# Optimization experiments

Measured on AMD Instinct MI355X. Metric: run time of the kernel, lower is better.

The kernel has to match this reference:

```python
import jax, jax.numpy as jnp
import numpy as np

TAU = 2.0
V_TH = 1.0
V_RESET = 0.0
BN_EPS = 1e-5
SG_ALPHA = 2.0  # spikingjelly ATan surrogate default

@jax.custom_vjp
def spike_fn(x):
    return (x >= 0.0).astype(x.dtype)

def _spike_fwd(x):
    return spike_fn(x), x

def _spike_bwd(x, g):
    # ATan surrogate: alpha/2 / (1 + (pi/2*alpha*x)^2)
    sg = (SG_ALPHA / 2.0) / (1.0 + (jnp.pi / 2.0 * SG_ALPHA * x) ** 2)
    return (g * sg,)

spike_fn.defvjp(_spike_fwd, _spike_bwd)

def lif_multistep(x_seq):
    # x_seq: [T, B, C]; decay_input=False, hard reset, detach_reset=True
    def step(v, xt):
        v = v - (v - V_RESET) / TAU + xt
        s = spike_fn(v - V_TH)
        sd = jax.lax.stop_gradient(s)
        v = (1.0 - sd) * v + sd * V_RESET
        return v, s
    v0 = jnp.zeros_like(x_seq[0])
    _, s_seq = jax.lax.scan(step, v0, x_seq)
    return s_seq

def bn_eval(x, gamma, beta, mean, var):
    # x: [T, B, C], normalize over channel C (eval-mode BN)
    inv = gamma * jax.lax.rsqrt(var + BN_EPS)
    return x * inv + (beta - mean * inv)

def setup_inputs() -> dict:
    key = jax.random.key(0)
    ks = jax.random.split(key, 8)
    B, T, Cin, C, K = 64, 200, 80, 1024, 7
    x = jax.random.normal(ks[0], (B, T, Cin), dtype=jnp.float32)
    pw_w = jax.random.normal(ks[1], (C, Cin), dtype=jnp.float32) * (1.0 / np.sqrt(Cin))
    pw_b = jnp.zeros((C,), dtype=jnp.float32)
    dw_w = jax.random.normal(ks[2], (C, K), dtype=jnp.float32) * (1.0 / np.sqrt(K))
    dw_b = jnp.zeros((C,), dtype=jnp.float32)
    bn1_gamma = jnp.ones((C,), dtype=jnp.float32)
    bn1_beta = jnp.zeros((C,), dtype=jnp.float32)
    bn1_mean = jnp.zeros((C,), dtype=jnp.float32)
    bn1_var = jnp.ones((C,), dtype=jnp.float32)
    lin_w = jax.random.normal(ks[3], (C, C), dtype=jnp.float32) * (1.0 / np.sqrt(C))
    bn2_gamma = jnp.ones((C,), dtype=jnp.float32)
    bn2_beta = jnp.zeros((C,), dtype=jnp.float32)
    bn2_mean = jnp.zeros((C,), dtype=jnp.float32)
    bn2_var = jnp.ones((C,), dtype=jnp.float32)
    return dict(x=x, pw_w=pw_w, pw_b=pw_b, dw_w=dw_w, dw_b=dw_b,
                bn1_gamma=bn1_gamma, bn1_beta=bn1_beta, bn1_mean=bn1_mean, bn1_var=bn1_var,
                lin_w=lin_w,
                bn2_gamma=bn2_gamma, bn2_beta=bn2_beta, bn2_mean=bn2_mean, bn2_var=bn2_var)

def reference(x, pw_w, pw_b, dw_w, dw_b,
              bn1_gamma, bn1_beta, bn1_mean, bn1_var,
              lin_w,
              bn2_gamma, bn2_beta, bn2_mean, bn2_var):
    # x: [B, T, Cin] -> trans1 -> [B, Cin, T]
    h = jnp.transpose(x, (0, 2, 1))
    # pointwise conv1d (kernel 1): [B, Cin, T] -> [B, C, T]
    h = jnp.einsum('bct,oc->bot', h, pw_w) + pw_b[None, :, None]
    # depthwise conv1d, kernel 7, same padding
    C = dw_w.shape[0]
    h = jax.lax.conv_general_dilated(
        h, dw_w[:, None, :], window_strides=(1,), padding=[(3, 3)],
        feature_group_count=C, dimension_numbers=('NCH', 'OIH', 'NCH'))
    h = h + dw_b[None, :, None]
    # trans2: [B, C, T] -> [T, B, C]
    h = jnp.transpose(h, (2, 0, 1))
    h = bn_eval(h, bn1_gamma, bn1_beta, bn1_mean, bn1_var)
    h = lif_multistep(h)
    # dropout1: eval mode -> identity
    h_res = h
    h = jnp.einsum('tbc,oc->tbo', h, lin_w)  # Linear, no bias
    h = bn_eval(h, bn2_gamma, bn2_beta, bn2_mean, bn2_var)
    h = lif_multistep(h)
    # dropout2: eval mode -> identity
    return h + h_res  # [T, B, C]
```

## Files before the change

### kernel.cpp

```cpp
#include <hip/hip_runtime.h>
#include <hip/hip_bf16.h>
#include <stdint.h>

#define B_    64
#define T_    200
#define CIN_  80
#define C_    1024
#define M_    (B_ * T_)
#define BCEL  (B_ * C_)

typedef __attribute__((ext_vector_type(4))) float f32x4;
typedef __attribute__((ext_vector_type(8))) _Float16 f16x8;
typedef __attribute__((ext_vector_type(4))) unsigned int u32x4;

__global__ __launch_bounds__(256) void gemm_abt(
    const float* __restrict__ A, const float* __restrict__ Bm,
    const float* __restrict__ bias, float* __restrict__ C,
    int M, int N, int K) {
  __shared__ float As[16][64];
  __shared__ float Bs[16][64];
  const int tid = threadIdx.x;
  const int tx = tid & 15;
  const int ty = tid >> 4;
  const int m0 = blockIdx.x * 64;
  const int n0 = blockIdx.y * 64;
  const int lr = tid >> 2;
  const int lc = (tid & 3) * 4;

  float acc[4][4] = {{0.f,0.f,0.f,0.f},{0.f,0.f,0.f,0.f},
                     {0.f,0.f,0.f,0.f},{0.f,0.f,0.f,0.f}};
  const float* Aro = A + (size_t)(m0 + lr) * K + lc;
  const float* Bro = Bm + (size_t)(n0 + lr) * K + lc;

  for (int k0 = 0; k0 < K; k0 += 16) {
    float4 a4 = *(const float4*)(Aro + k0);
    float4 b4 = *(const float4*)(Bro + k0);
    __syncthreads();
    As[lc + 0][lr] = a4.x; As[lc + 1][lr] = a4.y;
    As[lc + 2][lr] = a4.z; As[lc + 3][lr] = a4.w;
    Bs[lc + 0][lr] = b4.x; Bs[lc + 1][lr] = b4.y;
    Bs[lc + 2][lr] = b4.z; Bs[lc + 3][lr] = b4.w;
    __syncthreads();
#pragma unroll
    for (int kk = 0; kk < 16; ++kk) {
      float4 av = *(const float4*)&As[kk][ty * 4];
      float4 bv = *(const float4*)&Bs[kk][tx * 4];
      acc[0][0] = fmaf(av.x, bv.x, acc[0][0]);
      acc[0][1] = fmaf(av.x, bv.y, acc[0][1]);
      acc[0][2] = fmaf(av.x, bv.z, acc[0][2]);
      acc[0][3] = fmaf(av.x, bv.w, acc[0][3]);
      acc[1][0] = fmaf(av.y, bv.x, acc[1][0]);
      acc[1][1] = fmaf(av.y, bv.y, acc[1][1]);
      acc[1][2] = fmaf(av.y, bv.z, acc[1][2]);
      acc[1][3] = fmaf(av.y, bv.w, acc[1][3]);
      acc[2][0] = fmaf(av.z, bv.x, acc[2][0]);
      acc[2][1] = fmaf(av.z, bv.y, acc[2][1]);
      acc[2][2] = fmaf(av.z, bv.z, acc[2][2]);
      acc[2][3] = fmaf(av.z, bv.w, acc[2][3]);
      acc[3][0] = fmaf(av.w, bv.x, acc[3][0]);
      acc[3][1] = fmaf(av.w, bv.y, acc[3][1]);
      acc[3][2] = fmaf(av.w, bv.z, acc[3][2]);
      acc[3][3] = fmaf(av.w, bv.w, acc[3][3]);
    }
  }

  float bj[4] = {0.f, 0.f, 0.f, 0.f};
  if (bias) {
#pragma unroll
    for (int j = 0; j < 4; ++j) bj[j] = bias[n0 + tx * 4 + j];
  }
#pragma unroll
  for (int i = 0; i < 4; ++i) {
    int m = m0 + ty * 4 + i;
    float4 o4;
    o4.x = acc[i][0] + bj[0];
    o4.y = acc[i][1] + bj[1];
    o4.z = acc[i][2] + bj[2];
    o4.w = acc[i][3] + bj[3];
    *(float4*)&C[(size_t)m * N + n0 + tx * 4] = o4;
  }
}

__global__ __launch_bounds__(256) void dw_bn_lif(
    const float* __restrict__ p, const float* __restrict__ dw_w,
    const float* __restrict__ dw_b, const float* __restrict__ gam,
    const float* __restrict__ bet, const float* __restrict__ mu,
    const float* __restrict__ var, ushort* __restrict__ s1) {
  int gid = blockIdx.x * blockDim.x + threadIdx.x;
  int b = gid >> 10;
  int o = gid & 1023;

  float w[7];
#pragma unroll
  for (int k = 0; k < 7; ++k) w[k] = dw_w[o * 7 + k];
  float db = dw_b[o];
  float inv = (float)((double)gam[o] / sqrt((double)var[o] + 1e-5));
  float add = (float)((double)bet[o] - (double)mu[o] * (double)inv);

  const float* pp = p + (size_t)b * T_ * C_ + o;
  float win[14];
  win[0] = 0.f; win[1] = 0.f; win[2] = 0.f;
#pragma unroll
  for (int i = 0; i < 11; ++i) win[3 + i] = pp[(size_t)i * C_];

  float v = 0.f;
  size_t obase = (size_t)b * C_ + o;
  for (int c = 0; c < T_ / 8; ++c) {
    int t0 = c * 8;
    float nx[8];
#pragma unroll
    for (int j = 0; j < 8; ++j) {
      int tn = t0 + 11 + j;
      nx[j] = (tn < T_) ? pp[(size_t)tn * C_] : 0.f;
    }
#pragma unroll
    for (int s = 0; s < 8; ++s) {
      float u = db;
#pragma unroll
      for (int k = 0; k < 7; ++k) u = fmaf(w[k], win[s + k], u);
      u = fmaf(u, inv, add);
      v = fmaf(0.5f, v, u);
      bool sp = (v - 1.0f) >= 0.0f;
      s1[obase + (size_t)(t0 + s) * BCEL] = sp ? (ushort)0x3C00 : (ushort)0;
      v = sp ? 0.0f : v;
    }
#pragma unroll
    for (int i = 0; i < 6; ++i) win[i] = win[i + 8];
#pragma unroll
    for (int j = 0; j < 8; ++j) win[6 + j] = nx[j];
  }
}

__global__ __launch_bounds__(256) void split_w(
    const float* __restrict__ w, ushort* __restrict__ w0,
    ushort* __restrict__ w1, int n) {
  int i = blockIdx.x * 256 + threadIdx.x;
  if (i >= n) return;
  float x = w[i];
  union { _Float16 h; ushort u; } h0, h1;
  h0.h = (_Float16)x;
  if (fabsf(x) < 6.1035156e-5f) h0.u = 0;
  float r = x - (float)h0.h;
  h1.h = (_Float16)(r * 2048.0f);
  w0[i] = h0.u;
  w1[i] = h1.u;
}

#define BM 128
#define BN 128
#define BKg 32

__global__ __launch_bounds__(256) void gemm_mfma2(
    const ushort* __restrict__ A,
    const ushort* __restrict__ B0,
    const ushort* __restrict__ B1,
    float* __restrict__ Cout) {
  const int K = C_;
  const int N = C_;
  __shared__ __align__(16) ushort Ash[BM * BKg];
  __shared__ __align__(16) ushort Bsh[2][BN * BKg];

  const int tid  = threadIdx.x;
  const int lane = tid & 63;
  const int wm = ((tid >> 6) >> 1) * 64;
  const int wn = ((tid >> 6) & 1) * 64;

  int lin = blockIdx.x;
  int qq = gridDim.x >> 3;
  int wg = (lin & 7) * qq + (lin >> 3);
  const int m0 = (wg >> 3) * BM;
  const int n0 = (wg & 7) * BN;

  const int r0 = tid >> 2, kc0 = (tid & 3) * 8;
  const int r1 = (tid + 256) >> 2, kc1 = ((tid + 256) & 3) * 8;

  f32x4 acc[4][4] = {};

  for (int k0 = 0; k0 < K; k0 += BKg) {
    __syncthreads();
    {
      const ushort* s0 = A + (size_t)(m0 + r0) * K + k0 + kc0;
      const ushort* s1p = A + (size_t)(m0 + r1) * K + k0 + kc1;
      __builtin_amdgcn_global_load_lds(
          (const __attribute__((address_space(1))) uint32_t*)s0,
          (__attribute__((address_space(3))) uint32_t*)&Ash[tid * 8], 16, 0, 0);
      __builtin_amdgcn_global_load_lds(
          (const __attribute__((address_space(1))) uint32_t*)s1p,
          (__attribute__((address_space(3))) uint32_t*)&Ash[(tid + 256) * 8], 16, 0, 0);
    }
#pragma unroll
    for (int s = 0; s < 2; ++s) {
      const ushort* Bp = (s == 0) ? B0 : B1;
      const ushort* s0 = Bp + (size_t)(n0 + r0) * K + k0 + kc0;
      const ushort* s1p = Bp + (size_t)(n0 + r1) * K + k0 + kc1;
      __builtin_amdgcn_global_load_lds(
          (const __attribute__((address_space(1))) uint32_t*)s0,
          (__attribute__((address_space(3))) uint32_t*)&Bsh[s][tid * 8], 16, 0, 0);
      __builtin_amdgcn_global_load_lds(
          (const __attribute__((address_space(1))) uint32_t*)s1p,
          (__attribute__((address_space(3))) uint32_t*)&Bsh[s][(tid + 256) * 8], 16, 0, 0);
    }
    __syncthreads();

    const int fr = lane & 15;
    const int k8 = (lane >> 4) * 8;
    union HU { f16x8 h; u32x4 u; };
    f16x8 af[4], a2f[4];
#pragma unroll
    for (int m = 0; m < 4; ++m) {
      HU t;
      t.h = *(const f16x8*)&Ash[(wm + m * 16 + fr) * BKg + k8];
      af[m] = t.h;
      t.u &= 0x10001000u;
      a2f[m] = t.h;
    }
    f16x8 b0f[4], b1f[4];
#pragma unroll
    for (int n = 0; n < 4; ++n) {
      b0f[n] = *(const f16x8*)&Bsh[0][(wn + n * 16 + fr) * BKg + k8];
      b1f[n] = *(const f16x8*)&Bsh[1][(wn + n * 16 + fr) * BKg + k8];
    }
#pragma unroll
    for (int m = 0; m < 4; ++m)
#pragma unroll
      for (int n = 0; n < 4; ++n) {
        acc[m][n] = __builtin_amdgcn_mfma_f32_16x16x32_f16(
            af[m], b0f[n], acc[m][n], 0, 0, 0);
        acc[m][n] = __builtin_amdgcn_mfma_f32_16x16x32_f16(
            a2f[m], b1f[n], acc[m][n], 0, 0, 0);
      }
  }

  const int ccol = lane & 15;
  const int crow = (lane >> 4) * 4;
#pragma unroll
  for (int m = 0; m < 4; ++m)
#pragma unroll
    for (int n = 0; n < 4; ++n)
#pragma unroll
      for (int j = 0; j < 4; ++j) {
        int row = m0 + wm + m * 16 + crow + j;
        int col = n0 + wn + n * 16 + ccol;
        Cout[(size_t)row * N + col] = acc[m][n][j];
      }
}

__global__ __launch_bounds__(256) void bn_lif_add(
    const float* __restrict__ y, const ushort* __restrict__ s1b,
    const float* __restrict__ gam, const float* __restrict__ bet,
    const float* __restrict__ mu, const float* __restrict__ var,
    float* __restrict__ out) {
  int gid = blockIdx.x * blockDim.x + threadIdx.x;
  int o = gid & 1023;

  float inv = (float)((double)gam[o] / sqrt((double)var[o] + 1e-5));
  float add = (float)((double)bet[o] - (double)mu[o] * (double)inv);

  float v = 0.f;
  size_t base = (size_t)gid;
  float yv[8]; ushort sv[8];
#pragma unroll
  for (int j = 0; j < 8; ++j) {
    yv[j] = y[base + (size_t)j * BCEL];
    sv[j] = s1b[base + (size_t)j * BCEL];
  }
  for (int c = 0; c < T_ / 8; ++c) {
    int t0 = c * 8;
    float yn[8] = {0,0,0,0,0,0,0,0}; ushort sn[8] = {0,0,0,0,0,0,0,0};
    if (c + 1 < T_ / 8) {
#pragma unroll
      for (int j = 0; j < 8; ++j) {
        size_t idx = base + (size_t)(t0 + 8 + j) * BCEL;
        yn[j] = y[idx];
        sn[j] = s1b[idx];
      }
    }
#pragma unroll
    for (int j = 0; j < 8; ++j) {
      float u = fmaf(yv[j], inv, add);
      v = fmaf(0.5f, v, u);
      bool sp = (v - 1.0f) >= 0.0f;
      float s1v = sv[j] ? 1.0f : 0.0f;
      out[base + (size_t)(t0 + j) * BCEL] = (sp ? 1.0f : 0.0f) + s1v;
      v = sp ? 0.0f : v;
    }
#pragma unroll
    for (int j = 0; j < 8; ++j) { yv[j] = yn[j]; sv[j] = sn[j]; }
  }
}

extern "C" void kernel_launch(void* const* d_in, const int* in_sizes, int n_in,
                              void* d_out, int out_size, void* d_ws,
                              size_t ws_size, hipStream_t stream) {
  const float* x     = (const float*)d_in[0];
  const float* pw_w  = (const float*)d_in[1];
  const float* pw_b  = (const float*)d_in[2];
  const float* dw_w  = (const float*)d_in[3];
  const float* dw_b  = (const float*)d_in[4];
  const float* bn1g  = (const float*)d_in[5];
  const float* bn1b  = (const float*)d_in[6];
  const float* bn1m  = (const float*)d_in[7];
  const float* bn1v  = (const float*)d_in[8];
  const float* lin_w = (const float*)d_in[9];
  const float* bn2g  = (const float*)d_in[10];
  const float* bn2b  = (const float*)d_in[11];
  const float* bn2m  = (const float*)d_in[12];
  const float* bn2v  = (const float*)d_in[13];

  char* wsb  = (char*)d_ws;
  char* outb = (char*)d_out;
  const size_t PB  = (size_t)M_ * C_ * 4;
  const size_t SBB = (size_t)M_ * C_ * 2;
  const size_t WB  = (size_t)C_ * C_ * 2;

  float* p = (float*)d_ws;

  const bool primary = ws_size >= PB + SBB;
  ushort* spikes = primary ? (ushort*)(wsb + PB) : (ushort*)d_out;
  ushort* w0  = primary ? (ushort*)outb : (ushort*)(wsb + SBB);
  ushort* w1s = w0 + (size_t)C_ * C_;
  ushort* Sgemm = primary ? spikes : (ushort*)d_ws;
  float* ybuf = primary ? (float*)d_ws : (float*)d_out;

  dim3 pw_grid(M_ / 64, C_ / 64);
  gemm_abt<<<pw_grid, 256, 0, stream>>>(x, pw_w, pw_b, p, M_, C_, CIN_);

  dw_bn_lif<<<BCEL / 256, 256, 0, stream>>>(p, dw_w, dw_b, bn1g, bn1b, bn1m,
                                            bn1v, spikes);

  if (!primary)
    hipMemcpyAsync(d_ws, d_out, SBB, hipMemcpyDeviceToDevice, stream);

  split_w<<<(C_ * C_ + 255) / 256, 256, 0, stream>>>(lin_w, w0, w1s, C_ * C_);

  gemm_mfma2<<<(M_ / BM) * (C_ / BN), 256, 0, stream>>>(Sgemm, w0, w1s, ybuf);

  bn_lif_add<<<BCEL / 256, 256, 0, stream>>>(ybuf, Sgemm, bn2g, bn2b, bn2m,
                                             bn2v, (float*)d_out);
}
```

Baseline: 160.0 us.

## Double-buffer LDS in MFMA GEMM with XOR swizzle and prefetch in pointwise GEMM

The split-fp16 MFMA GEMM now uses two LDS buffers. It issues global-to-LDS loads for the next K tile before the MFMAs of the current tile, which removes one barrier per iteration and overlaps memory with compute. It also applies an XOR swizzle to the k offset on both the write and read side, meant to reduce LDS bank conflicts. The fp32 pointwise GEMM register-prefetches the next A/B float4 before the inner FMA loop. The cost is double the LDS footprint (48KB), which may limit occupancy.

```diff
diff --git a/kernel.cpp b/kernel.cpp
--- a/kernel.cpp
+++ b/kernel.cpp
@@ -32,15 +32,20 @@
   const float* Aro = A + (size_t)(m0 + lr) * K + lc;
   const float* Bro = Bm + (size_t)(n0 + lr) * K + lc;
 
+  float4 a4 = *(const float4*)(Aro);
+  float4 b4 = *(const float4*)(Bro);
+
   for (int k0 = 0; k0 < K; k0 += 16) {
-    float4 a4 = *(const float4*)(Aro + k0);
-    float4 b4 = *(const float4*)(Bro + k0);
     __syncthreads();
     As[lc + 0][lr] = a4.x; As[lc + 1][lr] = a4.y;
     As[lc + 2][lr] = a4.z; As[lc + 3][lr] = a4.w;
     Bs[lc + 0][lr] = b4.x; Bs[lc + 1][lr] = b4.y;
     Bs[lc + 2][lr] = b4.z; Bs[lc + 3][lr] = b4.w;
     __syncthreads();
+    if (k0 + 16 < K) {
+      a4 = *(const float4*)(Aro + k0 + 16);
+      b4 = *(const float4*)(Bro + k0 + 16);
+    }
 #pragma unroll
     for (int kk = 0; kk < 16; ++kk) {
       float4 av = *(const float4*)&As[kk][ty * 4];
@@ -150,15 +155,14 @@
 #define BN 128
 #define BKg 32
 
-__global__ __launch_bounds__(256) void gemm_mfma2(
+__global__ __launch_bounds__(256) void gemm_mfma2p(
     const ushort* __restrict__ A,
     const ushort* __restrict__ B0,
     const ushort* __restrict__ B1,
     float* __restrict__ Cout) {
   const int K = C_;
   const int N = C_;
-  __shared__ __align__(16) ushort Ash[BM * BKg];
-  __shared__ __align__(16) ushort Bsh[2][BN * BKg];
+  __shared__ __align__(16) ushort lds[2][3][BM * BKg];
 
   const int tid  = threadIdx.x;
   const int lane = tid & 63;
@@ -171,55 +175,59 @@
   const int m0 = (wg >> 3) * BM;
   const int n0 = (wg & 7) * BN;
 
-  const int r0 = tid >> 2, kc0 = (tid & 3) * 8;
-  const int r1 = (tid + 256) >> 2, kc1 = ((tid + 256) & 3) * 8;
+  const int r0 = tid >> 2, r1 = r0 + 64;
+  const int kc = (tid & 3) * 8;
+  const int ks = kc ^ (((tid >> 3) & 3) << 3);
+
+  const int fr = lane & 15;
+  const int k8 = (lane >> 4) * 8;
+  const int k8s = k8 ^ (((fr >> 1) & 3) << 3);
 
   f32x4 acc[4][4] = {};
 
+#define STAGE(bufi, kk0)                                                       \
+  do {                                                                         \
+    __builtin_amdgcn_global_load_lds(                                          \
+        (const __attribute__((address_space(1))) uint32_t*)(A + (size_t)(m0 + r0) * K + (kk0) + ks),  \
+        (__attribute__((address_space(3))) uint32_t*)&lds[bufi][0][tid * 8], 16, 0, 0);               \
+    __builtin_amdgcn_global_load_lds(                                          \
+        (const __attribute__((address_space(1))) uint32_t*)(A + (size_t)(m0 + r1) * K + (kk0) + ks),  \
+        (__attribute__((address_space(3))) uint32_t*)&lds[bufi][0][(tid + 256) * 8], 16, 0, 0);       \
+    __builtin_amdgcn_global_load_lds(                                          \
+        (const __attribute__((address_space(1))) uint32_t*)(B0 + (size_t)(n0 + r0) * K + (kk0) + ks), \
+        (__attribute__((address_space(3))) uint32_t*)&lds[bufi][1][tid * 8], 16, 0, 0);               \
+    __builtin_amdgcn_global_load_lds(                                          \
+        (const __attribute__((address_space(1))) uint32_t*)(B0 + (size_t)(n0 + r1) * K + (kk0) + ks), \
+        (__attribute__((address_space(3))) uint32_t*)&lds[bufi][1][(tid + 256) * 8], 16, 0, 0);       \
+    __builtin_amdgcn_global_load_lds(                                          \
+        (const __attribute__((address_space(1))) uint32_t*)(B1 + (size_t)(n0 + r0) * K + (kk0) + ks), \
+        (__attribute__((address_space(3))) uint32_t*)&lds[bufi][2][tid * 8], 16, 0, 0);               \
+    __builtin_amdgcn_global_load_lds(                                          \
+        (const __attribute__((address_space(1))) uint32_t*)(B1 + (size_t)(n0 + r1) * K + (kk0) + ks), \
+        (__attribute__((address_space(3))) uint32_t*)&lds[bufi][2][(tid + 256) * 8], 16, 0, 0);       \
+  } while (0)
+
+  STAGE(0, 0);
+  __syncthreads();
+
+  int buf = 0;
   for (int k0 = 0; k0 < K; k0 += BKg) {
-    __syncthreads();
-    {
-      const ushort* s0 = A + (size_t)(m0 + r0) * K + k0 + kc0;
-      const ushort* s1p = A + (size_t)(m0 + r1) * K + k0 + kc1;
-      __builtin_amdgcn_global_load_lds(
-          (const __attribute__((address_space(1))) uint32_t*)s0,
-          (__attribute__((address_space(3))) uint32_t*)&Ash[tid * 8], 16, 0, 0);
-      __builtin_amdgcn_global_load_lds(
-          (const __attribute__((address_space(1))) uint32_t*)s1p,
-          (__attribute__((address_space(3))) uint32_t*)&Ash[(tid + 256) * 8], 16, 0, 0);
-    }
-#pragma unroll
-    for (int s = 0; s < 2; ++s) {
-      const ushort* Bp = (s == 0) ? B0 : B1;
-      const ushort* s0 = Bp + (size_t)(n0 + r0) * K + k0 + kc0;
-      const ushort* s1p = Bp + (size_t)(n0 + r1) * K + k0 + kc1;
-      __builtin_amdgcn_global_load_lds(
-          (const __attribute__((address_space(1))) uint32_t*)s0,
-          (__attribute__((address_space(3))) uint32_t*)&Bsh[s][tid * 8], 16, 0, 0);
-      __builtin_amdgcn_global_load_lds(
-          (const __attribute__((address_space(1))) uint32_t*)s1p,
-          (__attribute__((address_space(3))) uint32_t*)&Bsh[s][(tid + 256) * 8], 16, 0, 0);
-    }
-    __syncthreads();
-
-    const int fr = lane & 15;
-    const int k8 = (lane >> 4) * 8;
     union HU { f16x8 h; u32x4 u; };
-    f16x8 af[4], a2f[4];
+    f16x8 af[4], a2f[4], b0f[4], b1f[4];
 #pragma unroll
     for (int m = 0; m < 4; ++m) {
       HU t;
-      t.h = *(const f16x8*)&Ash[(wm + m * 16 + fr) * BKg + k8];
+      t.h = *(const f16x8*)&lds[buf][0][(wm + m * 16 + fr) * BKg + k8s];
       af[m] = t.h;
       t.u &= 0x10001000u;
       a2f[m] = t.h;
     }
-    f16x8 b0f[4], b1f[4];
 #pragma unroll
     for (int n = 0; n < 4; ++n) {
-      b0f[n] = *(const f16x8*)&Bsh[0][(wn + n * 16 + fr) * BKg + k8];
-      b1f[n] = *(const f16x8*)&Bsh[1][(wn + n * 16 + fr) * BKg + k8];
-    }
+      b0f[n] = *(const f16x8*)&lds[buf][1][(wn + n * 16 + fr) * BKg + k8s];
+      b1f[n] = *(const f16x8*)&lds[buf][2][(wn + n * 16 + fr) * BKg + k8s];
+    }
+    if (k0 + BKg < K) STAGE(buf ^ 1, k0 + BKg);
 #pragma unroll
     for (int m = 0; m < 4; ++m)
 #pragma unroll
@@ -229,7 +237,10 @@
         acc[m][n] = __builtin_amdgcn_mfma_f32_16x16x32_f16(
             a2f[m], b1f[n], acc[m][n], 0, 0, 0);
       }
-  }
+    __syncthreads();
+    buf ^= 1;
+  }
+#undef STAGE
 
   const int ccol = lane & 15;
   const int crow = (lane >> 4) * 4;
@@ -311,7 +322,6 @@
   char* outb = (char*)d_out;
   const size_t PB  = (size_t)M_ * C_ * 4;
   const size_t SBB = (size_t)M_ * C_ * 2;
-  const size_t WB  = (size_t)C_ * C_ * 2;
 
   float* p = (float*)d_ws;
 
@@ -333,7 +343,7 @@
 
   split_w<<<(C_ * C_ + 255) / 256, 256, 0, stream>>>(lin_w, w0, w1s, C_ * C_);
 
-  gemm_mfma2<<<(M_ / BM) * (C_ / BN), 256, 0, stream>>>(Sgemm, w0, w1s, ybuf);
+  gemm_mfma2p<<<(M_ / BM) * (C_ / BN), 256, 0, stream>>>(Sgemm, w0, w1s, ybuf);
 
   bn_lif_add<<<BCEL / 256, 256, 0, stream>>>(ybuf, Sgemm, bn2g, bn2b, bn2m,
                                              bn2v, (float*)d_out);
```

Result: faster. 153.3 us (-4.2%).
